# Kernel optimization log

Hardware: AMD Instinct MI355X
Metric: run time of the kernel (lower is better)

## Reference

```python
import jax, jax.numpy as jnp
import numpy as np

LEVELS = [(128, 128), (64, 64), (32, 32), (16, 16)]  # (h, w) per level
NUM_HEADS = 8
NUM_LEVELS = 4
NUM_POINTS = 4
EMBED_DIMS = 256


def _bilinear_sample(img, gx, gy):
    """grid_sample(mode='bilinear', padding_mode='zeros', align_corners=False).
    img: (B, H, W, C); gx, gy: (B, N) in [-1, 1]. Returns (B, N, C)."""
    B, H, W, C = img.shape
    x = ((gx + 1.0) * W - 1.0) * 0.5
    y = ((gy + 1.0) * H - 1.0) * 0.5
    x0 = jnp.floor(x)
    y0 = jnp.floor(y)
    wx1 = x - x0
    wy1 = y - y0
    flat = img.reshape(B, H * W, C)

    def gather(xf, yf, w):
        xi = xf.astype(jnp.int32)
        yi = yf.astype(jnp.int32)
        valid = (xi >= 0) & (xi < W) & (yi >= 0) & (yi < H)
        idx = jnp.clip(yi, 0, H - 1) * W + jnp.clip(xi, 0, W - 1)
        v = jnp.take_along_axis(flat, idx[..., None], axis=1)
        return v * (w * valid)[..., None]

    return (gather(x0, y0, (1 - wx1) * (1 - wy1))
            + gather(x0 + 1, y0, wx1 * (1 - wy1))
            + gather(x0, y0 + 1, (1 - wx1) * wy1)
            + gather(x0 + 1, y0 + 1, wx1 * wy1))


def _msda(value, sampling_locations, attention_weights):
    """value: (bs, nv, nh, dh); sampling_locations: (bs, nq, nh, L, P, 2);
    attention_weights: (bs, nq, nh, L, P). Returns (bs, nq, nh*dh)."""
    bs, nv, nh, dh = value.shape
    nq = sampling_locations.shape[1]
    P = sampling_locations.shape[4]
    grids = 2.0 * sampling_locations - 1.0
    out = jnp.zeros((bs * nh, nq, dh), value.dtype)
    start = 0
    for l, (h, w) in enumerate(LEVELS):
        v = value[:, start:start + h * w]                      # (bs, h*w, nh, dh)
        start += h * w
        v = v.transpose(0, 2, 1, 3).reshape(bs * nh, h, w, dh)
        g = grids[:, :, :, l].transpose(0, 2, 1, 3, 4).reshape(bs * nh, nq * P, 2)
        s = _bilinear_sample(v, g[..., 0], g[..., 1]).reshape(bs * nh, nq, P, dh)
        wgt = attention_weights[:, :, :, l].transpose(0, 2, 1, 3).reshape(bs * nh, nq, P)
        out = out + jnp.einsum('bqpd,bqp->bqd', s, wgt)
    return out.reshape(bs, nh, nq, dh).transpose(0, 2, 1, 3).reshape(bs, nq, nh * dh)


def setup_inputs() -> dict:
    key = jax.random.key(0)
    ks = jax.random.split(key, 12)
    bs, nq, D = 2, sum(h * w for h, w in LEVELS), EMBED_DIMS
    spatial_shapes = jnp.array(LEVELS, dtype=jnp.int32)
    starts = np.cumsum([0] + [h * w for h, w in LEVELS[:-1]])
    return {
        'query': jax.random.normal(ks[0], (bs, nq, D), jnp.float32),
        'value': jax.random.normal(ks[1], (bs, nq, D), jnp.float32),
        'reference_points': jax.random.uniform(ks[2], (bs, nq, NUM_LEVELS, 2), jnp.float32),
        'spatial_shapes': spatial_shapes,
        'level_start_index': jnp.asarray(starts, dtype=jnp.int32),
        'Wv': jax.random.normal(ks[3], (D, D), jnp.float32) * 0.02,
        'bv': jnp.zeros((D,), jnp.float32),
        'Wo': jax.random.normal(ks[4], (D, NUM_HEADS * NUM_LEVELS * NUM_POINTS * 2), jnp.float32) * 0.02,
        'bo': jax.random.normal(ks[5], (NUM_HEADS * NUM_LEVELS * NUM_POINTS * 2,), jnp.float32) * 0.5,
        'Wa': jax.random.normal(ks[6], (D, NUM_HEADS * NUM_LEVELS * NUM_POINTS), jnp.float32) * 0.02,
        'ba': jnp.zeros((NUM_HEADS * NUM_LEVELS * NUM_POINTS,), jnp.float32),
        'Wout': jax.random.normal(ks[7], (D, D), jnp.float32) * 0.02,
        'bout': jnp.zeros((D,), jnp.float32),
    }


def reference(query, value, reference_points, spatial_shapes, level_start_index,
              Wv, bv, Wo, bo, Wa, ba, Wout, bout):
    bs, nq, D = query.shape
    nv = value.shape[1]
    nh, L, P = NUM_HEADS, NUM_LEVELS, NUM_POINTS
    dh = D // nh
    identity = query

    v = (value @ Wv + bv).reshape(bs, nv, nh, dh)
    offs = (query @ Wo + bo).reshape(bs, nq, nh, L, P, 2)
    attw = jax.nn.softmax((query @ Wa + ba).reshape(bs, nq, nh, L * P), axis=-1)
    attw = attw.reshape(bs, nq, nh, L, P)

    # offset_normalizer = (w, h) per level
    norm = jnp.stack([spatial_shapes[:, 1], spatial_shapes[:, 0]], -1).astype(query.dtype)
    sampling_locations = (reference_points[:, :, None, :, None, :]
                          + offs / norm[None, None, None, :, None, :])

    out = _msda(v, sampling_locations, attw)
    out = out @ Wout + bout
    return out + identity  # dropout is identity in eval
```

## Files before the change

kernel.cpp:

```cpp
#include <hip/hip_runtime.h>
#include <hip/hip_fp16.h>

#define BS 2
#define NQ 21760
#define NV 21760
#define DIM 256
#define NH 8
#define DH 32
#define NL 4
#define NP 4

typedef __attribute__((ext_vector_type(8))) _Float16 f16x8;
typedef __attribute__((ext_vector_type(4))) float f32x4;

__device__ __forceinline__ unsigned short f2h(float f) {
    return __half_as_ushort(__float2half(f));
}
__device__ __forceinline__ float h2f(unsigned short s) {
    return __half2float(__ushort_as_half(s));
}

__global__ __launch_bounds__(64) void k_wprep(
    const float* __restrict__ Wo, const float* __restrict__ Wa,
    const float* __restrict__ Wv, const float* __restrict__ Wout,
    unsigned short* __restrict__ wsw)
{
    const int tile = blockIdx.x;
    const int lane = threadIdx.x;
    const float* W; int N, nb, kb;
    if (tile < 192) { nb = tile >> 3; kb = tile & 7;
        if (nb < 16) { W = Wo; N = 256; } else { W = Wa; N = 128; nb -= 16; } }
    else if (tile < 320) { int tt = tile - 192; nb = tt >> 3; kb = tt & 7; W = Wv;   N = 256; }
    else               { int tt = tile - 320; nb = tt >> 3; kb = tt & 7; W = Wout; N = 256; }
    const int quad = lane >> 4, l15 = lane & 15;
    const int col = nb * 16 + l15;
    unsigned int pk[4];
#pragma unroll
    for (int jj = 0; jj < 4; jj++) {
        int k0 = kb * 32 + quad * 8 + jj * 2;
        pk[jj] = (unsigned int)f2h(W[(size_t)k0 * N + col])
               | ((unsigned int)f2h(W[(size_t)(k0 + 1) * N + col]) << 16);
    }
    *(uint4*)(wsw + (size_t)tile * 512 + lane * 8) = *(const uint4*)pk;
}

__device__ __forceinline__ void stage32_f32(const float* __restrict__ src,
                                            unsigned short* __restrict__ As)
{
    const int t = threadIdx.x;
    const int colg = t & 63;
    const int row0 = t >> 6;
#pragma unroll
    for (int i = 0; i < 8; i++) {
        int row = row0 + i * 4;
        float4 f = ((const float4*)(src + (size_t)row * 256))[colg];
        uint2 p;
        p.x = (unsigned int)f2h(f.x) | ((unsigned int)f2h(f.y) << 16);
        p.y = (unsigned int)f2h(f.z) | ((unsigned int)f2h(f.w) << 16);
        *(uint2*)&As[row * 264 + colg * 4] = p;
    }
}
__device__ __forceinline__ void stage32_h16(const unsigned short* __restrict__ src,
                                            unsigned short* __restrict__ As)
{
    const int t = threadIdx.x;
    const int colg = t & 63;
    const int row0 = t >> 6;
#pragma unroll
    for (int i = 0; i < 8; i++) {
        int row = row0 + i * 4;
        uint2 u = ((const uint2*)(src + (size_t)row * 256))[colg];
        *(uint2*)&As[row * 264 + colg * 4] = u;
    }
}

template<int M>
__device__ __forceinline__ void gemm32(const unsigned short* __restrict__ As,
                                       const unsigned short* __restrict__ wswb,
                                       int mt0, f32x4 acc[][2], int lane)
{
    const int quad = lane >> 4, l15 = lane & 15;
#pragma unroll
    for (int kh = 0; kh < 2; kh++) {
        f16x8 aw[M][4];
#pragma unroll
        for (int m = 0; m < M; m++)
#pragma unroll
            for (int j = 0; j < 4; j++)
                aw[m][j] = *(const f16x8*)(wswb +
                    ((((mt0 + m) * 8 + kh * 4 + j) << 9) + (lane << 3)));
#pragma unroll
        for (int j = 0; j < 4; j++) {
            const int kb = kh * 4 + j;
            f16x8 dq[2];
#pragma unroll
            for (int n = 0; n < 2; n++)
                dq[n] = *(const f16x8*)&As[(n * 16 + l15) * 264 + kb * 32 + quad * 8];
#pragma unroll
            for (int m = 0; m < M; m++)
#pragma unroll
                for (int n = 0; n < 2; n++)
                    acc[m][n] = __builtin_amdgcn_mfma_f32_16x16x32_f16(aw[m][j], dq[n], acc[m][n], 0, 0, 0);
        }
    }
}

__global__ __launch_bounds__(256) void k_proj(
    const float* __restrict__ value,
    const float* __restrict__ query,
    const float* __restrict__ refp,
    const unsigned short* __restrict__ wsw,
    const float* __restrict__ bv,
    const float* __restrict__ bo,
    const float* __restrict__ ba,
    unsigned short* __restrict__ v_hm,
    float* __restrict__ locs_ws,
    unsigned short* __restrict__ attw_b)
{
    __shared__ unsigned short As[32 * 264];
    const int t = threadIdx.x;
    const int w = t >> 6, lane = t & 63;
    const int quad = lane >> 4, l15 = lane & 15;

    if (blockIdx.x < 1360) {
        const int tile = blockIdx.x;
        const int r0i = tile * 32;
        const int bb = (tile >= 680);
        const int pix0 = r0i - bb * NV;
        stage32_f32(value + (size_t)r0i * 256, As);
        __syncthreads();
        f32x4 acc[4][2];
#pragma unroll
        for (int m = 0; m < 4; m++)
#pragma unroll
            for (int n = 0; n < 2; n++) acc[m][n] = (f32x4){0.f, 0.f, 0.f, 0.f};
        gemm32<4>(As, wsw + 98304, w * 4, acc, lane);
#pragma unroll
        for (int m = 0; m < 4; m++) {
            const int col = w * 64 + m * 16 + quad * 4;
            const int h = col >> 5, ch = col & 31;
            const float4 bias = *(const float4*)(bv + col);
            unsigned short* __restrict__ vh =
                v_hm + ((size_t)(bb * NH + h) * NV + pix0) * DH + ch;
#pragma unroll
            for (int n = 0; n < 2; n++) {
                f32x4 a = acc[m][n];
                uint2 o;
                o.x = (unsigned int)f2h(a[0] + bias.x)
                    | ((unsigned int)f2h(a[1] + bias.y) << 16);
                o.y = (unsigned int)f2h(a[2] + bias.z)
                    | ((unsigned int)f2h(a[3] + bias.w) << 16);
                *(uint2*)(vh + (size_t)(n * 16 + l15) * DH) = o;
            }
        }
    } else {
        const int qb = blockIdx.x - 1360;
        const int rt = qb >> 1, ch2 = qb & 1;
        const size_t r0 = (size_t)rt * 32;
        stage32_f32(query + r0 * 256, As);
        __syncthreads();
        f32x4 acc[3][2];
#pragma unroll
        for (int m = 0; m < 3; m++)
#pragma unroll
            for (int n = 0; n < 2; n++) acc[m][n] = (f32x4){0.f, 0.f, 0.f, 0.f};
        const int mt0 = ch2 * 12 + w * 3;
        gemm32<3>(As, wsw, mt0, acc, lane);
#pragma unroll
        for (int m = 0; m < 3; m++) {
            const int mt = mt0 + m;
            if (mt < 16) {
                const int c0 = mt * 16 + quad * 4;
                const int l = (c0 >> 3) & 3;
                const float rnorm = 1.f / (float)(128 >> l);
                const float4 bias = *(const float4*)(bo + c0);
#pragma unroll
                for (int n = 0; n < 2; n++) {
                    size_t row = r0 + n * 16 + l15;
                    float2 ref = *(const float2*)(refp + row * 8 + l * 2);
                    f32x4 a = acc[m][n];
                    float4 o;
                    o.x = ref.x + (a[0] + bias.x) * rnorm;
                    o.y = ref.y + (a[1] + bias.y) * rnorm;
                    o.z = ref.x + (a[2] + bias.z) * rnorm;
                    o.w = ref.y + (a[3] + bias.w) * rnorm;
                    *(float4*)(locs_ws + row * 256 + c0) = o;
                }
            } else {
                const int c0 = (mt - 16) * 16 + quad * 4;
                const float4 bias = *(const float4*)(ba + c0);
#pragma unroll
                for (int n = 0; n < 2; n++) {
                    size_t row = r0 + n * 16 + l15;
                    f32x4 a = acc[m][n];
                    float v0 = a[0] + bias.x, v1 = a[1] + bias.y;
                    float v2 = a[2] + bias.z, v3 = a[3] + bias.w;
                    float mm = fmaxf(fmaxf(v0, v1), fmaxf(v2, v3));
                    mm = fmaxf(mm, __shfl_xor(mm, 16, 64));
                    mm = fmaxf(mm, __shfl_xor(mm, 32, 64));
                    float e0 = __expf(v0 - mm), e1 = __expf(v1 - mm);
                    float e2 = __expf(v2 - mm), e3 = __expf(v3 - mm);
                    float s = (e0 + e1) + (e2 + e3);
                    s += __shfl_xor(s, 16, 64);
                    s += __shfl_xor(s, 32, 64);
                    float rs = 1.f / s;
                    uint2 o;
                    o.x = (unsigned int)f2h(e0 * rs) | ((unsigned int)f2h(e1 * rs) << 16);
                    o.y = (unsigned int)f2h(e2 * rs) | ((unsigned int)f2h(e3 * rs) << 16);
                    *(uint2*)(attw_b + row * 128 + c0) = o;
                }
            }
        }
    }
}

__device__ __forceinline__ void acc8(float wf, uint4 d, float* ac)
{
    __half2 p0 = *(__half2*)&d.x;
    __half2 p1 = *(__half2*)&d.y;
    __half2 p2 = *(__half2*)&d.z;
    __half2 p3 = *(__half2*)&d.w;
    ac[0] = fmaf(wf, __half2float(__low2half(p0)),  ac[0]);
    ac[1] = fmaf(wf, __half2float(__high2half(p0)), ac[1]);
    ac[2] = fmaf(wf, __half2float(__low2half(p1)),  ac[2]);
    ac[3] = fmaf(wf, __half2float(__high2half(p1)), ac[3]);
    ac[4] = fmaf(wf, __half2float(__low2half(p2)),  ac[4]);
    ac[5] = fmaf(wf, __half2float(__high2half(p2)), ac[5]);
    ac[6] = fmaf(wf, __half2float(__low2half(p3)),  ac[6]);
    ac[7] = fmaf(wf, __half2float(__high2half(p3)), ac[7]);
}

__global__ __launch_bounds__(256) void k_sample(
    const unsigned short* __restrict__ v_hm,
    const float* __restrict__ locs_ws,
    const unsigned short* __restrict__ attw_b,
    unsigned short* __restrict__ msda_ws)
{
    __shared__ uint4 tap[16 * 2 * 33];
    const int t = threadIdx.x;
    const int bid = blockIdx.x;

    const int xcd  = bid & 7;
    const int slot = bid >> 3;
    const int sub  = (slot >= 680) ? 1 : 0;
    const int chunk = slot - sub * 680;
    const int pair = xcd * 2 + sub;
    const int b = pair & 1;
    const int h = pair >> 1;
    const int q0 = chunk * 32;

#pragma unroll
    for (int i = 0; i < 2; i++) {
        const int item = t + i * 256;
        const int tp = item & 15;
        const int q  = item >> 4;
        const size_t row = (size_t)(b * NQ + q0 + q);
        float2 xy = *(const float2*)(locs_ws + row * 256 + h * 32 + tp * 2);
        float a   = h2f(attw_b[row * 128 + h * 16 + tp]);

        const int l = tp >> 2;
        const int Wl = 128 >> l;
        const float Wf = (float)Wl;
        const int start = (l == 0) ? 0 : (l == 1) ? 16384 : (l == 2) ? 20480 : 21504;
        float x = xy.x * Wf - 0.5f;
        float y = xy.y * Wf - 0.5f;
        float xf = floorf(x), yf = floorf(y);
        int x0 = (int)xf, y0 = (int)yf;
        float wx1 = x - xf, wx0 = 1.f - wx1;
        float wy1 = y - yf, wy0 = 1.f - wy1;
        const int base = min(max(x0, 0), Wl - 2);
        const int sh = x0 - base;
        const float wxA = (sh == 0) ? wx0 : (sh == -1) ? wx1 : 0.f;
        const float wxB = (sh == 0) ? wx1 : (sh == 1)  ? wx0 : 0.f;
#pragma unroll
        for (int dy = 0; dy < 2; dy++) {
            int yi = y0 + dy;
            bool yv = (yi >= 0) && (yi < Wl);
            int yc = min(max(yi, 0), Wl - 1);
            float wY = yv ? a * (dy ? wy1 : wy0) : 0.f;
            uint4 rec;
            rec.x = __float_as_uint(wY * wxA);
            rec.y = __float_as_uint(wY * wxB);
            rec.z = (unsigned int)(start + yc * Wl + base) * 64u;
            rec.w = 0u;
            tap[(tp * 2 + dy) * 33 + q] = rec;
        }
    }
    __syncthreads();

    const int w4   = t >> 6;
    const int lane = t & 63;
    const int ql   = lane >> 3;
    const int g    = lane & 7;
    const int q    = w4 * 8 + ql;
    const bool selA = (g < 4);
    const unsigned int goff = (unsigned int)g * 16u;
    const char* __restrict__ vb =
        (const char*)(v_hm + (size_t)(b * NH + h) * NV * DH);

    float ac[8] = {0.f, 0.f, 0.f, 0.f, 0.f, 0.f, 0.f, 0.f};
#pragma unroll
    for (int it = 0; it < 32; it++) {
        uint4 rec = tap[it * 33 + q];
        float wf = __uint_as_float(selA ? rec.x : rec.y);
        uint4 d = *(const uint4*)(vb + (rec.z + goff));
        acc8(wf, d, ac);
    }
#pragma unroll
    for (int k = 0; k < 8; k++) ac[k] += __shfl_xor(ac[k], 4, 64);
    if (selA) {
        uint4 o;
        o.x = (unsigned int)f2h(ac[0]) | ((unsigned int)f2h(ac[1]) << 16);
        o.y = (unsigned int)f2h(ac[2]) | ((unsigned int)f2h(ac[3]) << 16);
        o.z = (unsigned int)f2h(ac[4]) | ((unsigned int)f2h(ac[5]) << 16);
        o.w = (unsigned int)f2h(ac[6]) | ((unsigned int)f2h(ac[7]) << 16);
        *(uint4*)(msda_ws + (size_t)(b * NQ + q0 + q) * DIM + h * DH + g * 8) = o;
    }
}

__global__ __launch_bounds__(256) void k_out_mfma(
    const unsigned short* __restrict__ msda_ws,
    const unsigned short* __restrict__ wswo,
    const float* __restrict__ bout,
    const float* __restrict__ query,
    float* __restrict__ out)
{
    __shared__ unsigned short As[32 * 264];
    const int t = threadIdx.x;
    const int w = t >> 6, lane = t & 63;
    const int quad = lane >> 4, l15 = lane & 15;
    const size_t r0 = (size_t)blockIdx.x * 32;

    stage32_h16(msda_ws + r0 * 256, As);
    __syncthreads();

    f32x4 acc[4][2];
#pragma unroll
    for (int m = 0; m < 4; m++)
#pragma unroll
        for (int n = 0; n < 2; n++) acc[m][n] = (f32x4){0.f, 0.f, 0.f, 0.f};
    gemm32<4>(As, wswo, w * 4, acc, lane);

#pragma unroll
    for (int m = 0; m < 4; m++) {
        const int c0 = w * 64 + m * 16 + quad * 4;
        const float4 bias = *(const float4*)(bout + c0);
#pragma unroll
        for (int n = 0; n < 2; n++) {
            size_t row = r0 + n * 16 + l15;
            float4 q4 = *(const float4*)(query + row * 256 + c0);
            f32x4 a = acc[m][n];
            float4 o;
            o.x = a[0] + bias.x + q4.x;
            o.y = a[1] + bias.y + q4.y;
            o.z = a[2] + bias.z + q4.z;
            o.w = a[3] + bias.w + q4.w;
            *(float4*)(out + row * 256 + c0) = o;
        }
    }
}

extern "C" void kernel_launch(void* const* d_in, const int* in_sizes, int n_in,
                              void* d_out, int out_size, void* d_ws, size_t ws_size,
                              hipStream_t stream)
{
    const float* query = (const float*)d_in[0];
    const float* value = (const float*)d_in[1];
    const float* refp  = (const float*)d_in[2];
    const float* Wv   = (const float*)d_in[5];
    const float* bv   = (const float*)d_in[6];
    const float* Wo   = (const float*)d_in[7];
    const float* bo   = (const float*)d_in[8];
    const float* Wa   = (const float*)d_in[9];
    const float* ba   = (const float*)d_in[10];
    const float* Wout = (const float*)d_in[11];
    const float* bout = (const float*)d_in[12];
    float* out = (float*)d_out;

    char* ws = (char*)d_ws;
    unsigned short* v_hm = (unsigned short*)ws;    ws += (size_t)BS * NH * NV * DH * 2;
    float* locs_ws = (float*)ws;                   ws += (size_t)BS * NQ * DIM * 4;
    unsigned short* attw_b = (unsigned short*)ws;  ws += (size_t)BS * NQ * 128 * 2;
    unsigned short* msda_ws = (unsigned short*)ws; ws += (size_t)BS * NQ * DIM * 2;
    unsigned short* wsw = (unsigned short*)ws;

    k_wprep   <<<448, 64,  0, stream>>>(Wo, Wa, Wv, Wout, wsw);
    k_proj    <<<4080, 256, 0, stream>>>(value, query, refp, wsw, bv, bo, ba,
                                         v_hm, locs_ws, attw_b);
    k_sample  <<<10880, 256, 0, stream>>>(v_hm, locs_ws, attw_b, msda_ws);
    k_out_mfma<<<1360, 256, 0, stream>>>(msda_ws, wsw + 163840, bout, query, out);
}
```

Measured before the change: 266.0 us.

## Process two tiles per block with register prefetch and half-precision sampling accumulation

The projection and output GEMM kernels now handle two 32-row tiles per block, prefetching the second tile into registers while the first is computed, which halves grid size and lets query blocks do both column halves from one staged tile. The sampling kernel stores bilinear weights as packed fp16 and accumulates with packed half2 FMAs instead of fp32 FMAs. This cuts staging loads and conversion work, but fp16 accumulation over 32 taps reduces numerical precision and may exceed tolerance.

```diff
diff --git a/kernel.cpp b/kernel.cpp
--- a/kernel.cpp
+++ b/kernel.cpp
@@ -72,6 +72,46 @@
         uint2 u = ((const uint2*)(src + (size_t)row * 256))[colg];
         *(uint2*)&As[row * 264 + colg * 4] = u;
     }
+}
+__device__ __forceinline__ void pf_load32_f32(const float* __restrict__ src, float4* pf)
+{
+    const int t = threadIdx.x;
+    const int colg = t & 63;
+    const int row0 = t >> 6;
+#pragma unroll
+    for (int i = 0; i < 8; i++)
+        pf[i] = ((const float4*)(src + (size_t)(row0 + i * 4) * 256))[colg];
+}
+__device__ __forceinline__ void pf_store32_f32(const float4* pf, unsigned short* __restrict__ As)
+{
+    const int t = threadIdx.x;
+    const int colg = t & 63;
+    const int row0 = t >> 6;
+#pragma unroll
+    for (int i = 0; i < 8; i++) {
+        uint2 p;
+        p.x = (unsigned int)f2h(pf[i].x) | ((unsigned int)f2h(pf[i].y) << 16);
+        p.y = (unsigned int)f2h(pf[i].z) | ((unsigned int)f2h(pf[i].w) << 16);
+        *(uint2*)&As[(row0 + i * 4) * 264 + colg * 4] = p;
+    }
+}
+__device__ __forceinline__ void pf_load32_h16(const unsigned short* __restrict__ src, uint2* pf)
+{
+    const int t = threadIdx.x;
+    const int colg = t & 63;
+    const int row0 = t >> 6;
+#pragma unroll
+    for (int i = 0; i < 8; i++)
+        pf[i] = ((const uint2*)(src + (size_t)(row0 + i * 4) * 256))[colg];
+}
+__device__ __forceinline__ void pf_store32_h16(const uint2* pf, unsigned short* __restrict__ As)
+{
+    const int t = threadIdx.x;
+    const int colg = t & 63;
+    const int row0 = t >> 6;
+#pragma unroll
+    for (int i = 0; i < 8; i++)
+        *(uint2*)&As[(row0 + i * 4) * 264 + colg * 4] = pf[i];
 }
 
 template<int M>
@@ -122,112 +162,118 @@
     const int w = t >> 6, lane = t & 63;
     const int quad = lane >> 4, l15 = lane & 15;
 
-    if (blockIdx.x < 1360) {
-        const int tile = blockIdx.x;
-        const int r0i = tile * 32;
-        const int bb = (tile >= 680);
-        const int pix0 = r0i - bb * NV;
-        stage32_f32(value + (size_t)r0i * 256, As);
+    if (blockIdx.x < 680) {
+        const int tb = blockIdx.x * 2;
+        stage32_f32(value + (size_t)tb * 32 * 256, As);
         __syncthreads();
-        f32x4 acc[4][2];
-#pragma unroll
-        for (int m = 0; m < 4; m++)
-#pragma unroll
-            for (int n = 0; n < 2; n++) acc[m][n] = (f32x4){0.f, 0.f, 0.f, 0.f};
-        gemm32<4>(As, wsw + 98304, w * 4, acc, lane);
-#pragma unroll
-        for (int m = 0; m < 4; m++) {
-            const int col = w * 64 + m * 16 + quad * 4;
-            const int h = col >> 5, ch = col & 31;
-            const float4 bias = *(const float4*)(bv + col);
-            unsigned short* __restrict__ vh =
-                v_hm + ((size_t)(bb * NH + h) * NV + pix0) * DH + ch;
-#pragma unroll
-            for (int n = 0; n < 2; n++) {
-                f32x4 a = acc[m][n];
-                uint2 o;
-                o.x = (unsigned int)f2h(a[0] + bias.x)
-                    | ((unsigned int)f2h(a[1] + bias.y) << 16);
-                o.y = (unsigned int)f2h(a[2] + bias.z)
-                    | ((unsigned int)f2h(a[3] + bias.w) << 16);
-                *(uint2*)(vh + (size_t)(n * 16 + l15) * DH) = o;
-            }
-        }
-    } else {
-        const int qb = blockIdx.x - 1360;
-        const int rt = qb >> 1, ch2 = qb & 1;
-        const size_t r0 = (size_t)rt * 32;
-        stage32_f32(query + r0 * 256, As);
-        __syncthreads();
-        f32x4 acc[3][2];
-#pragma unroll
-        for (int m = 0; m < 3; m++)
-#pragma unroll
-            for (int n = 0; n < 2; n++) acc[m][n] = (f32x4){0.f, 0.f, 0.f, 0.f};
-        const int mt0 = ch2 * 12 + w * 3;
-        gemm32<3>(As, wsw, mt0, acc, lane);
-#pragma unroll
-        for (int m = 0; m < 3; m++) {
-            const int mt = mt0 + m;
-            if (mt < 16) {
-                const int c0 = mt * 16 + quad * 4;
-                const int l = (c0 >> 3) & 3;
-                const float rnorm = 1.f / (float)(128 >> l);
-                const float4 bias = *(const float4*)(bo + c0);
+        float4 pf[8];
+        pf_load32_f32(value + (size_t)(tb + 1) * 32 * 256, pf);
+#pragma unroll
+        for (int tt = 0; tt < 2; tt++) {
+            const int tile = tb + tt;
+            const int bb = (tile >= 680);
+            const int pix0 = tile * 32 - bb * NV;
+            f32x4 acc[4][2];
+#pragma unroll
+            for (int m = 0; m < 4; m++)
+#pragma unroll
+                for (int n = 0; n < 2; n++) acc[m][n] = (f32x4){0.f, 0.f, 0.f, 0.f};
+            gemm32<4>(As, wsw + 98304, w * 4, acc, lane);
+#pragma unroll
+            for (int m = 0; m < 4; m++) {
+                const int col = w * 64 + m * 16 + quad * 4;
+                const int h = col >> 5, ch = col & 31;
+                const float4 bias = *(const float4*)(bv + col);
+                unsigned short* __restrict__ vh =
+                    v_hm + ((size_t)(bb * NH + h) * NV + pix0) * DH + ch;
 #pragma unroll
                 for (int n = 0; n < 2; n++) {
-                    size_t row = r0 + n * 16 + l15;
-                    float2 ref = *(const float2*)(refp + row * 8 + l * 2);
                     f32x4 a = acc[m][n];
-                    float4 o;
-                    o.x = ref.x + (a[0] + bias.x) * rnorm;
-                    o.y = ref.y + (a[1] + bias.y) * rnorm;
-                    o.z = ref.x + (a[2] + bias.z) * rnorm;
-                    o.w = ref.y + (a[3] + bias.w) * rnorm;
-                    *(float4*)(locs_ws + row * 256 + c0) = o;
-                }
-            } else {
-                const int c0 = (mt - 16) * 16 + quad * 4;
-                const float4 bias = *(const float4*)(ba + c0);
-#pragma unroll
-                for (int n = 0; n < 2; n++) {
-                    size_t row = r0 + n * 16 + l15;
-                    f32x4 a = acc[m][n];
-                    float v0 = a[0] + bias.x, v1 = a[1] + bias.y;
-                    float v2 = a[2] + bias.z, v3 = a[3] + bias.w;
-                    float mm = fmaxf(fmaxf(v0, v1), fmaxf(v2, v3));
-                    mm = fmaxf(mm, __shfl_xor(mm, 16, 64));
-                    mm = fmaxf(mm, __shfl_xor(mm, 32, 64));
-                    float e0 = __expf(v0 - mm), e1 = __expf(v1 - mm);
-                    float e2 = __expf(v2 - mm), e3 = __expf(v3 - mm);
-                    float s = (e0 + e1) + (e2 + e3);
-                    s += __shfl_xor(s, 16, 64);
-                    s += __shfl_xor(s, 32, 64);
-                    float rs = 1.f / s;
                     uint2 o;
-                    o.x = (unsigned int)f2h(e0 * rs) | ((unsigned int)f2h(e1 * rs) << 16);
-                    o.y = (unsigned int)f2h(e2 * rs) | ((unsigned int)f2h(e3 * rs) << 16);
-                    *(uint2*)(attw_b + row * 128 + c0) = o;
+                    o.x = (unsigned int)f2h(a[0] + bias.x)
+                        | ((unsigned int)f2h(a[1] + bias.y) << 16);
+                    o.y = (unsigned int)f2h(a[2] + bias.z)
+                        | ((unsigned int)f2h(a[3] + bias.w) << 16);
+                    *(uint2*)(vh + (size_t)(n * 16 + l15) * DH) = o;
                 }
             }
-        }
-    }
-}
-
-__device__ __forceinline__ void acc8(float wf, uint4 d, float* ac)
-{
-    __half2 p0 = *(__half2*)&d.x;
-    __half2 p1 = *(__half2*)&d.y;
-    __half2 p2 = *(__half2*)&d.z;
-    __half2 p3 = *(__half2*)&d.w;
-    ac[0] = fmaf(wf, __half2float(__low2half(p0)),  ac[0]);
-    ac[1] = fmaf(wf, __half2float(__high2half(p0)), ac[1]);
-    ac[2] = fmaf(wf, __half2float(__low2half(p1)),  ac[2]);
-    ac[3] = fmaf(wf, __half2float(__high2half(p1)), ac[3]);
-    ac[4] = fmaf(wf, __half2float(__low2half(p2)),  ac[4]);
-    ac[5] = fmaf(wf, __half2float(__high2half(p2)), ac[5]);
-    ac[6] = fmaf(wf, __half2float(__low2half(p3)),  ac[6]);
-    ac[7] = fmaf(wf, __half2float(__high2half(p3)), ac[7]);
+            if (tt == 0) {
+                __syncthreads();
+                pf_store32_f32(pf, As);
+                __syncthreads();
+            }
+        }
+    } else {
+        const int tb = (blockIdx.x - 680) * 2;
+        stage32_f32(query + (size_t)tb * 32 * 256, As);
+        __syncthreads();
+        float4 pf[8];
+        pf_load32_f32(query + (size_t)(tb + 1) * 32 * 256, pf);
+#pragma unroll
+        for (int tt = 0; tt < 2; tt++) {
+            const size_t r0 = (size_t)(tb + tt) * 32;
+#pragma unroll
+            for (int pass = 0; pass < 2; pass++) {
+                const int mt0 = pass * 12 + w * 3;
+                f32x4 acc[3][2];
+#pragma unroll
+                for (int m = 0; m < 3; m++)
+#pragma unroll
+                    for (int n = 0; n < 2; n++) acc[m][n] = (f32x4){0.f, 0.f, 0.f, 0.f};
+                gemm32<3>(As, wsw, mt0, acc, lane);
+#pragma unroll
+                for (int m = 0; m < 3; m++) {
+                    const int mt = mt0 + m;
+                    if (mt < 16) {
+                        const int c0 = mt * 16 + quad * 4;
+                        const int l = (c0 >> 3) & 3;
+                        const float rnorm = 1.f / (float)(128 >> l);
+                        const float4 bias = *(const float4*)(bo + c0);
+#pragma unroll
+                        for (int n = 0; n < 2; n++) {
+                            size_t row = r0 + n * 16 + l15;
+                            float2 ref = *(const float2*)(refp + row * 8 + l * 2);
+                            f32x4 a = acc[m][n];
+                            float4 o;
+                            o.x = ref.x + (a[0] + bias.x) * rnorm;
+                            o.y = ref.y + (a[1] + bias.y) * rnorm;
+                            o.z = ref.x + (a[2] + bias.z) * rnorm;
+                            o.w = ref.y + (a[3] + bias.w) * rnorm;
+                            *(float4*)(locs_ws + row * 256 + c0) = o;
+                        }
+                    } else {
+                        const int c0 = (mt - 16) * 16 + quad * 4;
+                        const float4 bias = *(const float4*)(ba + c0);
+#pragma unroll
+                        for (int n = 0; n < 2; n++) {
+                            size_t row = r0 + n * 16 + l15;
+                            f32x4 a = acc[m][n];
+                            float v0 = a[0] + bias.x, v1 = a[1] + bias.y;
+                            float v2 = a[2] + bias.z, v3 = a[3] + bias.w;
+                            float mm = fmaxf(fmaxf(v0, v1), fmaxf(v2, v3));
+                            mm = fmaxf(mm, __shfl_xor(mm, 16, 64));
+                            mm = fmaxf(mm, __shfl_xor(mm, 32, 64));
+                            float e0 = __expf(v0 - mm), e1 = __expf(v1 - mm);
+                            float e2 = __expf(v2 - mm), e3 = __expf(v3 - mm);
+                            float s = (e0 + e1) + (e2 + e3);
+                            s += __shfl_xor(s, 16, 64);
+                            s += __shfl_xor(s, 32, 64);
+                            float rs = 1.f / s;
+                            uint2 o;
+                            o.x = (unsigned int)f2h(e0 * rs) | ((unsigned int)f2h(e1 * rs) << 16);
+                            o.y = (unsigned int)f2h(e2 * rs) | ((unsigned int)f2h(e3 * rs) << 16);
+                            *(uint2*)(attw_b + row * 128 + c0) = o;
+                        }
+                    }
+                }
+            }
+            if (tt == 0) {
+                __syncthreads();
+                pf_store32_f32(pf, As);
+                __syncthreads();
+            }
+        }
+    }
 }
 
 __global__ __launch_bounds__(256) void k_sample(
@@ -278,9 +324,11 @@
             bool yv = (yi >= 0) && (yi < Wl);
             int yc = min(max(yi, 0), Wl - 1);
             float wY = yv ? a * (dy ? wy1 : wy0) : 0.f;
+            unsigned short ha = f2h(wY * wxA);
+            unsigned short hb = f2h(wY * wxB);
             uint4 rec;
-            rec.x = __float_as_uint(wY * wxA);
-            rec.y = __float_as_uint(wY * wxB);
+            rec.x = (unsigned int)ha | ((unsigned int)ha << 16);
+            rec.y = (unsigned int)hb | ((unsigned int)hb << 16);
             rec.z = (unsigned int)(start + yc * Wl + base) * 64u;
             rec.w = 0u;
             tap[(tp * 2 + dy) * 33 + q] = rec;
@@ -298,22 +346,32 @@
     const char* __restrict__ vb =
         (const char*)(v_hm + (size_t)(b * NH + h) * NV * DH);
 
-    float ac[8] = {0.f, 0.f, 0.f, 0.f, 0.f, 0.f, 0.f, 0.f};
+    __half2 a2[4];
+#pragma unroll
+    for (int k = 0; k < 4; k++) a2[k] = __half2half2(__ushort_as_half(0));
 #pragma unroll
     for (int it = 0; it < 32; it++) {
         uint4 rec = tap[it * 33 + q];
-        float wf = __uint_as_float(selA ? rec.x : rec.y);
+        unsigned int wsel = selA ? rec.x : rec.y;
+        __half2 w2 = *(__half2*)&wsel;
         uint4 d = *(const uint4*)(vb + (rec.z + goff));
-        acc8(wf, d, ac);
-    }
-#pragma unroll
-    for (int k = 0; k < 8; k++) ac[k] += __shfl_xor(ac[k], 4, 64);
+        a2[0] = __hfma2(w2, *(__half2*)&d.x, a2[0]);
+        a2[1] = __hfma2(w2, *(__half2*)&d.y, a2[1]);
+        a2[2] = __hfma2(w2, *(__half2*)&d.z, a2[2]);
+        a2[3] = __hfma2(w2, *(__half2*)&d.w, a2[3]);
+    }
+#pragma unroll
+    for (int k = 0; k < 4; k++) {
+        unsigned int u = *(unsigned int*)&a2[k];
+        unsigned int v = __shfl_xor(u, 4, 64);
+        a2[k] = __hadd2(a2[k], *(__half2*)&v);
+    }
     if (selA) {
         uint4 o;
-        o.x = (unsigned int)f2h(ac[0]) | ((unsigned int)f2h(ac[1]) << 16);
-        o.y = (unsigned int)f2h(ac[2]) | ((unsigned int)f2h(ac[3]) << 16);
-        o.z = (unsigned int)f2h(ac[4]) | ((unsigned int)f2h(ac[5]) << 16);
-        o.w = (unsigned int)f2h(ac[6]) | ((unsigned int)f2h(ac[7]) << 16);
+        o.x = *(unsigned int*)&a2[0];
+        o.y = *(unsigned int*)&a2[1];
+        o.z = *(unsigned int*)&a2[2];
+        o.w = *(unsigned int*)&a2[3];
         *(uint4*)(msda_ws + (size_t)(b * NQ + q0 + q) * DIM + h * DH + g * 8) = o;
     }
 }
@@ -329,33 +387,43 @@
     const int t = threadIdx.x;
     const int w = t >> 6, lane = t & 63;
     const int quad = lane >> 4, l15 = lane & 15;
-    const size_t r0 = (size_t)blockIdx.x * 32;
-
-    stage32_h16(msda_ws + r0 * 256, As);
+    const int tb = blockIdx.x * 2;
+
+    stage32_h16(msda_ws + (size_t)tb * 32 * 256, As);
     __syncthreads();
-
-    f32x4 acc[4][2];
-#pragma unroll
-    for (int m = 0; m < 4; m++)
-#pragma unroll
-        for (int n = 0; n < 2; n++) acc[m][n] = (f32x4){0.f, 0.f, 0.f, 0.f};
-    gemm32<4>(As, wswo, w * 4, acc, lane);
-
-#pragma unroll
-    for (int m = 0; m < 4; m++) {
-        const int c0 = w * 64 + m * 16 + quad * 4;
-        const float4 bias = *(const float4*)(bout + c0);
-#pragma unroll
-        for (int n = 0; n < 2; n++) {
-            size_t row = r0 + n * 16 + l15;
-            float4 q4 = *(const float4*)(query + row * 256 + c0);
-            f32x4 a = acc[m][n];
-            float4 o;
-            o.x = a[0] + bias.x + q4.x;
-            o.y = a[1] + bias.y + q4.y;
-            o.z = a[2] + bias.z + q4.z;
-            o.w = a[3] + bias.w + q4.w;
-            *(float4*)(out + row * 256 + c0) = o;
+    uint2 pf[8];
+    pf_load32_h16(msda_ws + (size_t)(tb + 1) * 32 * 256, pf);
+
+#pragma unroll
+    for (int tt = 0; tt < 2; tt++) {
+        const size_t r0 = (size_t)(tb + tt) * 32;
+        f32x4 acc[4][2];
+#pragma unroll
+        for (int m = 0; m < 4; m++)
+#pragma unroll
+            for (int n = 0; n < 2; n++) acc[m][n] = (f32x4){0.f, 0.f, 0.f, 0.f};
+        gemm32<4>(As, wswo, w * 4, acc, lane);
+#pragma unroll
+        for (int m = 0; m < 4; m++) {
+            const int c0 = w * 64 + m * 16 + quad * 4;
+            const float4 bias = *(const float4*)(bout + c0);
+#pragma unroll
+            for (int n = 0; n < 2; n++) {
+                size_t row = r0 + n * 16 + l15;
+                float4 q4 = *(const float4*)(query + row * 256 + c0);
+                f32x4 a = acc[m][n];
+                float4 o;
+                o.x = a[0] + bias.x + q4.x;
+                o.y = a[1] + bias.y + q4.y;
+                o.z = a[2] + bias.z + q4.z;
+                o.w = a[3] + bias.w + q4.w;
+                *(float4*)(out + row * 256 + c0) = o;
+            }
+        }
+        if (tt == 0) {
+            __syncthreads();
+            pf_store32_h16(pf, As);
+            __syncthreads();
         }
     }
 }
@@ -385,8 +453,8 @@
     unsigned short* wsw = (unsigned short*)ws;
 
     k_wprep   <<<448, 64,  0, stream>>>(Wo, Wa, Wv, Wout, wsw);
-    k_proj    <<<4080, 256, 0, stream>>>(value, query, refp, wsw, bv, bo, ba,
+    k_proj    <<<1360, 256, 0, stream>>>(value, query, refp, wsw, bv, bo, ba,
                                          v_hm, locs_ws, attw_b);
     k_sample  <<<10880, 256, 0, stream>>>(v_hm, locs_ws, attw_b, msda_ws);
-    k_out_mfma<<<1360, 256, 0, stream>>>(msda_ws, wsw + 163840, bout, query, out);
-}
+    k_out_mfma<<<680, 256, 0, stream>>>(msda_ws, wsw + 163840, bout, query, out);
+}
```

After: 276.4 us. +3.9%, slower.
